# Kernel tuning notes

Hardware: AMD Instinct MI355X
Metric: run time of the kernel (lower is better)

## Reference

```python
import jax, jax.numpy as jnp
import numpy as np

# Qwen3-Next GatedDeltaNet dims (tp_size = 1)
H = 2048          # hidden_size
HK, HV = 16, 32   # num_k_heads, num_v_heads
G = HV // HK      # v-heads per k-head
DK, DV = 128, 128 # head_k_dim, head_v_dim
KEY_DIM = HK * DK        # 2048
VAL_DIM = HV * DV        # 4096
CONV_DIM = 2 * KEY_DIM + VAL_DIM   # 8192
QKVZ = 2 * KEY_DIM + 2 * VAL_DIM   # 12288
BA = 2 * HV
K = 4             # conv kernel size
L = 4096          # tokens (one prefill sequence)
EPS = 1e-6


def setup_inputs() -> dict:
    key = jax.random.key(0)
    ks = jax.random.split(key, 5)
    s = lambda k, shape, sc: jax.random.normal(k, shape, jnp.float32) * sc
    return {
        'hidden_states': s(ks[0], (L, H), 1.0),
        'in_proj_w': s(ks[1], (H, QKVZ + BA), H ** -0.5),
        'conv_w': s(ks[2], (CONV_DIM, K), 0.25),
        'A_log': jnp.zeros((HV,), jnp.float32),
        'dt_bias': jnp.ones((HV,), jnp.float32),
        'norm_w': jnp.ones((DV,), jnp.float32),
        'out_proj_w': s(ks[3], (VAL_DIM, H), VAL_DIM ** -0.5),
    }


def _l2norm(x):
    return x * jax.lax.rsqrt(jnp.sum(x * x, axis=-1, keepdims=True) + EPS)


def _gdn_forward(hidden_states, in_proj_w, conv_w, A_log, dt_bias, norm_w, out_proj_w):
    # in_proj -> split qkvz / ba, fix_query_key_value_ordering
    proj = hidden_states @ in_proj_w                       # [L, QKVZ+BA]
    qkvz, ba = proj[:, :QKVZ], proj[:, QKVZ:]
    qkvz = qkvz.reshape(L, HK, 2 * DK + 2 * G * DV)        # per-k-head layout
    q = qkvz[:, :, :DK]                                    # [L,HK,DK]
    k = qkvz[:, :, DK:2 * DK]                              # [L,HK,DK]
    v = qkvz[:, :, 2 * DK:2 * DK + G * DV].reshape(L, HV, DV)
    z = qkvz[:, :, 2 * DK + G * DV:].reshape(L, HV, DV)
    ba = ba.reshape(L, HK, 2 * G)
    b = ba[:, :, :G].reshape(L, HV)
    a = ba[:, :, G:].reshape(L, HV)

    # depthwise causal conv1d over time (kernel K, left pad K-1) + silu
    mixed_qkv = jnp.concatenate(
        [q.reshape(L, KEY_DIM), k.reshape(L, KEY_DIM), v.reshape(L, VAL_DIM)], axis=-1)
    xp = jnp.pad(mixed_qkv, ((K - 1, 0), (0, 0)))
    conv_out = sum(conv_w[:, j] * xp[j:j + L] for j in range(K))
    mixed_qkv = jax.nn.silu(conv_out)

    q = mixed_qkv[:, :KEY_DIM].reshape(L, HK, DK)
    k = mixed_qkv[:, KEY_DIM:2 * KEY_DIM].reshape(L, HK, DK)
    v = mixed_qkv[:, 2 * KEY_DIM:].reshape(L, HV, DV)

    # gating: beta = sigmoid(b); g = -exp(A_log) * softplus(a + dt_bias)
    beta = jax.nn.sigmoid(b)                               # [L,HV]
    g = -jnp.exp(A_log) * jax.nn.softplus(a + dt_bias)     # [L,HV] (log decay)

    # expand k-heads to v-heads, qk l2-norm, scale q
    q = jnp.repeat(q, G, axis=1)                           # [L,HV,DK]
    k = jnp.repeat(k, G, axis=1)
    q = _l2norm(q) * (DK ** -0.5)
    k = _l2norm(k)

    # gated delta rule recurrence over time (state S: [HV, DK, DV])
    def step(S, inp):
        q_t, k_t, v_t, g_t, b_t = inp
        S = S * jnp.exp(g_t)[:, None, None]
        delta = (v_t - jnp.einsum('hk,hkv->hv', k_t, S)) * b_t[:, None]
        S = S + jnp.einsum('hk,hv->hkv', k_t, delta)
        o = jnp.einsum('hk,hkv->hv', q_t, S)
        return S, o

    S0 = jnp.zeros((HV, DK, DV), jnp.float32)
    _, core = jax.lax.scan(step, S0, (q, k, v, g, beta))   # core: [L,HV,DV]

    # gated RMSNorm (norm before gate): RMSNorm(x)*w*silu(z)
    var = jnp.mean(core * core, axis=-1, keepdims=True)
    core = core * jax.lax.rsqrt(var + EPS) * norm_w
    core = core * jax.nn.silu(z)

    return core.reshape(L, VAL_DIM) @ out_proj_w           # [L, H]


def reference(hidden_states, in_proj_w, conv_w, A_log, dt_bias, norm_w, out_proj_w):
    return _gdn_forward(hidden_states, in_proj_w, conv_w, A_log, dt_bias, norm_w, out_proj_w)
```

## Files before the change

### kernel.cpp

```cpp
#include <hip/hip_runtime.h>
#include <hip/hip_bf16.h>

#define L_SEQ 4096
#define HDIM 2048
#define NPROJA 8256
#define NPACK 12352
#define WLD 12352
#define EPS_ 1e-6f

using bf16 = __hip_bfloat16;
typedef __attribute__((ext_vector_type(8))) short short8;
typedef __attribute__((ext_vector_type(4))) float f32x4;

__device__ __forceinline__ float b2f(bf16 x) { return __bfloat162float(x); }
__device__ __forceinline__ bf16 f2b(float x) { return __float2bfloat16(x); }
__device__ __forceinline__ unsigned short b2u(bf16 x) {
  union { bf16 b; unsigned short u; } c; c.b = x; return c.u;
}
__device__ __forceinline__ void* swz(void* base, int row, int rowbytes, int colbyte) {
  return (void*)((char*)base + row * rowbytes + (colbyte ^ ((row & 7) << 4)));
}
__device__ __forceinline__ const void* swzc(const void* base, int row, int rowbytes, int colbyte) {
  return (const void*)((const char*)base + row * rowbytes + (colbyte ^ ((row & 7) << 4)));
}
__device__ __forceinline__ void* swzk(void* base, int row, int colbyte) {
  return (void*)((char*)base + row * 128 + (colbyte ^ (((row >> 3) & 7) << 4)));
}
__device__ __forceinline__ const void* swzkc(const void* base, int row, int colbyte) {
  return (const void*)((const char*)base + row * 128 + (colbyte ^ (((row >> 3) & 7) << 4)));
}

__device__ __forceinline__ void async_copy16(const void* g, void* l) {
  __builtin_amdgcn_global_load_lds(
      (const __attribute__((address_space(1))) void*)g,
      (__attribute__((address_space(3))) void*)l, 16, 0, 0);
}

__global__ __launch_bounds__(256) void cvt_bf16(const float* __restrict__ in,
                                                bf16* __restrict__ outp) {
  int i = (blockIdx.x * 256 + threadIdx.x) * 4;
  float4 v = *(const float4*)&in[i];
  bf16 o4[4] = {f2b(v.x), f2b(v.y), f2b(v.z), f2b(v.w)};
  *(ushort4*)&outp[i] = *(ushort4*)o4;
}

template <int MODE>
__device__ __forceinline__ int pmap(int n) {
  if constexpr (MODE == 3) {
    if (n < 2048) return (n >> 7) * 768 + (n & 127);
    else if (n < 4096) { int m = n - 2048; return (m >> 7) * 768 + 128 + (m & 127); }
    else if (n < 8192) { int m = n - 4096; return (m >> 8) * 768 + 256 + (m & 255); }
    else if (n < 8256) return 12288 + (n - 8192);
    else { int m = n - 8256; return (m >> 8) * 768 + 512 + (m & 255); }
  } else {
    return n;
  }
}

template <int MODE>
__global__ __launch_bounds__(256) void transpose_w(
    const float* __restrict__ W, bf16* __restrict__ Bt, int ldw, int Kd) {
  __shared__ float T[64][65];
  const int nb = blockIdx.x * 64, kb = blockIdx.y * 64;
  const int tid = threadIdx.x;
  const int c = tid & 63, gq = tid >> 6;
  const int sbase = pmap<MODE>(nb);
#pragma unroll
  for (int i = 0; i < 16; ++i) {
    int r = gq * 16 + i;
    T[c][r] = W[(size_t)(kb + r) * ldw + sbase + c];
  }
  __syncthreads();
#pragma unroll
  for (int i = 0; i < 16; ++i) {
    int n = gq * 16 + i;
    Bt[(size_t)(nb + n) * Kd + kb + c] = f2b(T[n][c]);
  }
}

template <int ROUTE>
__global__ __launch_bounds__(256) void gemm_bt(
    const bf16* __restrict__ A, const bf16* __restrict__ Bt,
    void* __restrict__ Cp, bf16* __restrict__ Cz, int N, int Kd,
    int MBnum, int NBnum) {
  __shared__ bf16 As[2][128 * 32];
  __shared__ bf16 Bs[2][128 * 32];
  const int tid = threadIdx.x;
  const int wave = tid >> 6, lane = tid & 63;
  const int l15 = lane & 15, quad = lane >> 4;

  int m_blk, n_blk;
  {
    const int CW = 32;
    int fullc = NBnum / CW;
    int rem = NBnum - fullc * CW;
    int thr = fullc * CW * MBnum;
    int wg = blockIdx.x;
    if (wg < thr) {
      int cw = CW * MBnum;
      int chunk = wg / cw, w = wg - chunk * cw;
      n_blk = chunk * CW + (w & (CW - 1));
      m_blk = w / CW;
    } else {
      int w2 = wg - thr;
      int r = rem ? rem : 1;
      n_blk = fullc * CW + w2 % r;
      m_blk = w2 / r;
    }
  }
  const int m0 = m_blk * 128, n0 = n_blk * 128;
  const int mw = (wave >> 1) * 64, nw = (wave & 1) * 64;

  f32x4 acc[4][4];
#pragma unroll
  for (int i = 0; i < 4; i++)
#pragma unroll
    for (int j = 0; j < 4; j++) acc[i][j] = {0.f, 0.f, 0.f, 0.f};

  const bf16* a_src0 = A + (size_t)(m0 + (tid >> 2)) * Kd + (tid & 3) * 8;
  const bf16* a_src1 = a_src0 + (size_t)64 * Kd;
  const bf16* b_src0 = Bt + (size_t)(n0 + (tid >> 2)) * Kd + (tid & 3) * 8;
  const bf16* b_src1 = b_src0 + (size_t)64 * Kd;
  const int d0 = tid * 8, d1 = (tid + 256) * 8;

  async_copy16(a_src0, &As[0][d0]);
  async_copy16(a_src1, &As[0][d1]);
  async_copy16(b_src0, &Bs[0][d0]);
  async_copy16(b_src1, &Bs[0][d1]);

  int cur = 0;
  for (int k0 = 0; k0 < Kd; k0 += 32, cur ^= 1) {
    __syncthreads();
    if (k0 + 32 < Kd) {
      const int nk = k0 + 32, nb = cur ^ 1;
      async_copy16(a_src0 + nk, &As[nb][d0]);
      async_copy16(a_src1 + nk, &As[nb][d1]);
      async_copy16(b_src0 + nk, &Bs[nb][d0]);
      async_copy16(b_src1 + nk, &Bs[nb][d1]);
    }
    short8 af[4], bfr[4];
#pragma unroll
    for (int i = 0; i < 4; i++)
      af[i] = *(const short8*)&As[cur][(mw + i * 16 + l15) * 32 + quad * 8];
#pragma unroll
    for (int j = 0; j < 4; j++)
      bfr[j] = *(const short8*)&Bs[cur][(nw + j * 16 + l15) * 32 + quad * 8];
#pragma unroll
    for (int i = 0; i < 4; i++)
#pragma unroll
      for (int j = 0; j < 4; j++)
        acc[i][j] = __builtin_amdgcn_mfma_f32_16x16x32_bf16(af[i], bfr[j],
                                                            acc[i][j], 0, 0, 0);
  }

#pragma unroll
  for (int i = 0; i < 4; i++) {
#pragma unroll
    for (int j = 0; j < 4; j++) {
      int col = n0 + nw + j * 16 + l15;
      if (col < N) {
#pragma unroll
        for (int r = 0; r < 4; r++) {
          int row = m0 + mw + i * 16 + quad * 4 + r;
          if (ROUTE == 0) {
            ((float*)Cp)[(size_t)row * N + col] = acc[i][j][r];
          } else {
            if (col < NPROJA)
              ((bf16*)Cp)[(size_t)row * NPROJA + col] = f2b(acc[i][j][r]);
            else
              Cz[(size_t)row * 4096 + (col - NPROJA)] = f2b(acc[i][j][r]);
          }
        }
      }
    }
  }
}

__global__ __launch_bounds__(128) void conv_norm_qk(
    const bf16* __restrict__ proj, const float* __restrict__ conv_w,
    bf16* __restrict__ qn, bf16* __restrict__ kn) {
  const int t = blockIdx.x >> 4, hk = blockIdx.x & 15;
  const int d = threadIdx.x;
  const int cq = hk * 128 + d;
  const int ck = 2048 + hk * 128 + d;
  float sq = 0.f, sk = 0.f;
#pragma unroll
  for (int j = 0; j < 4; j++) {
    int ts = t + j - 3;
    if (ts >= 0) {
      sq += conv_w[cq * 4 + j] * b2f(proj[(size_t)ts * NPROJA + cq]);
      sk += conv_w[ck * 4 + j] * b2f(proj[(size_t)ts * NPROJA + ck]);
    }
  }
  float qv = sq / (1.f + expf(-sq));
  float kv = sk / (1.f + expf(-sk));
  float ssq = qv * qv, ssk = kv * kv;
#pragma unroll
  for (int off = 32; off > 0; off >>= 1) {
    ssq += __shfl_down(ssq, off, 64);
    ssk += __shfl_down(ssk, off, 64);
  }
  __shared__ float red[4];
  if ((d & 63) == 0) {
    red[(d >> 6) * 2] = ssq;
    red[(d >> 6) * 2 + 1] = ssk;
  }
  __syncthreads();
  float sumq = red[0] + red[2];
  float sumk = red[1] + red[3];
  size_t o = (size_t)(t * 16 + hk) * 128 + d;
  qn[o] = f2b(qv * rsqrtf(sumq + EPS_) * 0.08838834764831845f);
  kn[o] = f2b(kv * rsqrtf(sumk + EPS_));
}

__global__ __launch_bounds__(256) void conv_silu_v(
    const bf16* __restrict__ proj, const float* __restrict__ conv_w,
    bf16* __restrict__ vbuf) {
  int idx = blockIdx.x * 256 + threadIdx.x;
  int t = idx >> 12, c = idx & 4095;
  int chan = 4096 + c;
  float s = 0.f;
#pragma unroll
  for (int j = 0; j < 4; j++) {
    int ts = t + j - 3;
    if (ts >= 0) s += conv_w[chan * 4 + j] * b2f(proj[(size_t)ts * NPROJA + chan]);
  }
  vbuf[idx] = f2b(s / (1.f + expf(-s)));
}

__global__ __launch_bounds__(256) void compute_bg(
    const bf16* __restrict__ proj, const float* __restrict__ A_log,
    const float* __restrict__ dt_bias, float* __restrict__ beta_arr,
    float* __restrict__ g_arr) {
  int idx = blockIdx.x * 256 + threadIdx.x;
  int t = idx >> 5, hv = idx & 31;
  size_t base = (size_t)t * NPROJA + 8192 + (hv >> 1) * 4 + (hv & 1);
  float b = b2f(proj[base]);
  float a = b2f(proj[base + 2]);
  beta_arr[idx] = 1.f / (1.f + expf(-b));
  float x = a + dt_bias[hv];
  float sp = (x > 20.f) ? x : log1pf(expf(x));
  g_arr[idx] = -expf(A_log[hv]) * sp;
}

__global__ __launch_bounds__(512) void precompute_chunk(
    const bf16* __restrict__ kn, const bf16* __restrict__ vbuf,
    const float* __restrict__ g_arr, const float* __restrict__ beta_arr,
    bf16* __restrict__ TV, bf16* __restrict__ TK) {
  const int c = blockIdx.x >> 5, h = blockIdx.x & 31, hk = h >> 1;
  const int t0 = c * 64, tid = threadIdx.x;
  __shared__ float Kf[64][129];
  __shared__ float X[64][256];
  __shared__ float BA[64][64];
  __shared__ float cgs[64], bet[64], eKs[64];

  for (int e = tid; e < 1024; e += 512) {
    int row = e >> 4, s = e & 15;
    short8 v = *(const short8*)(kn + ((size_t)(t0 + row) * 16 + hk) * 128 + s * 8);
    bf16 tmp[8];
    *(short8*)tmp = v;
#pragma unroll
    for (int k = 0; k < 8; ++k) Kf[row][s * 8 + k] = b2f(tmp[k]);
  }
  if (tid < 64) {
    float bb = beta_arr[(size_t)(t0 + tid) * 32 + h];
    bet[tid] = bb;
    float x = g_arr[(size_t)(t0 + tid) * 32 + h];
#pragma unroll
    for (int off = 1; off < 64; off <<= 1) {
      float o = __shfl_up(x, off, 64);
      if (tid >= off) x += o;
    }
    cgs[tid] = x;
    eKs[tid] = bb * expf(x);
  }
  __syncthreads();
  for (int e = tid; e < 8192; e += 512) {
    int i = e >> 7, d = e & 127;
    X[i][d] = bet[i] * b2f(vbuf[(size_t)(t0 + i) * 4096 + h * 128 + d]);
    X[i][128 + d] = eKs[i] * Kf[i][d];
  }
  {
    const int ti = tid >> 4, tj = tid & 15;
    float acc[2][4];
#pragma unroll
    for (int r = 0; r < 2; ++r)
#pragma unroll
      for (int s = 0; s < 4; ++s) acc[r][s] = 0.f;
    for (int dk = 0; dk < 128; ++dk) {
      float a0 = Kf[ti * 2 + 0][dk], a1 = Kf[ti * 2 + 1][dk];
      float c0 = Kf[tj * 4 + 0][dk], c1 = Kf[tj * 4 + 1][dk];
      float c2 = Kf[tj * 4 + 2][dk], c3 = Kf[tj * 4 + 3][dk];
      acc[0][0] += a0 * c0; acc[0][1] += a0 * c1; acc[0][2] += a0 * c2; acc[0][3] += a0 * c3;
      acc[1][0] += a1 * c0; acc[1][1] += a1 * c1; acc[1][2] += a1 * c2; acc[1][3] += a1 * c3;
    }
#pragma unroll
    for (int r = 0; r < 2; ++r)
#pragma unroll
      for (int s = 0; s < 4; ++s) {
        int i = ti * 2 + r, j = tj * 4 + s;
        BA[i][j] = (j < i) ? bet[i] * expf(cgs[i] - cgs[j]) * acc[r][s] : 0.f;
      }
  }
  __syncthreads();
  if (tid < 256) {
    const int d = tid;
    for (int i = 1; i < 64; ++i) {
      const float* bar = BA[i];
      float s0 = 0.f, s1 = 0.f;
      int j = 0;
      for (; j + 1 < i; j += 2) {
        s0 += bar[j] * X[j][d];
        s1 += bar[j + 1] * X[j + 1][d];
      }
      if (j < i) s0 += bar[j] * X[j][d];
      X[i][d] -= s0 + s1;
    }
  }
  __syncthreads();
  for (int e = tid; e < 8192; e += 512) {
    int i = e >> 7, d = e & 127;
    size_t o = ((size_t)(t0 + i) * 32 + h) * 128 + d;
    TV[o] = f2b(X[i][d]);
    TK[o] = f2b(X[i][128 + d]);
  }
}

__global__ __launch_bounds__(512) void seq_kernel(
    bf16* TVU,
    const bf16* __restrict__ TKg, const bf16* __restrict__ qn,
    const bf16* __restrict__ kn, const float* __restrict__ g_arr,
    bf16* __restrict__ Oin) {
  const int h = blockIdx.x >> 1, dvh = blockIdx.x & 1, hk = h >> 1;
  const int dv0 = dvh * 64;
  const int tid = threadIdx.x;
  const int wave = tid >> 6, lane = tid & 63, l15 = lane & 15, quad = lane >> 4;
  const int mi = wave >> 1, half = wave & 1;
  const int srow = tid >> 4, scol = tid & 15;

  __shared__ bf16 STh[64 * 128], STl[64 * 128];
  __shared__ bf16 UTh[64 * 64], UTl[64 * 64];
  __shared__ bf16 TKs[64 * 128];
  __shared__ bf16 Qts[64 * 128];
  __shared__ bf16 KhT[128 * 64];

  for (int e = tid; e < 4096; e += 512) {
    ((unsigned int*)STh)[e] = 0u;
    ((unsigned int*)STl)[e] = 0u;
  }
  f32x4 Sf[4];
#pragma unroll
  for (int i = 0; i < 4; i++) Sf[i] = {0.f, 0.f, 0.f, 0.f};

  short8 tkr0, tkr1, qr0, qr1, kr0, kr1;
  float gv;
  auto issue_loads = [&](int c) {
    const size_t t0 = (size_t)c << 6;
    tkr0 = *(const short8*)(TKg + ((t0 + srow) * 32 + h) * 128 + scol * 8);
    tkr1 = *(const short8*)(TKg + ((t0 + 32 + srow) * 32 + h) * 128 + scol * 8);
    qr0 = *(const short8*)(qn + ((t0 + srow) * 16 + hk) * 128 + scol * 8);
    qr1 = *(const short8*)(qn + ((t0 + 32 + srow) * 16 + hk) * 128 + scol * 8);
    kr0 = *(const short8*)(kn + ((t0 + srow) * 16 + hk) * 128 + scol * 8);
    kr1 = *(const short8*)(kn + ((t0 + 32 + srow) * 16 + hk) * 128 + scol * 8);
    gv = g_arr[(t0 + lane) * 32 + h];
  };
  issue_loads(0);

  for (int c = 0; c < 64; ++c) {
    const int t0 = c << 6;
    __syncthreads();

    bf16 tvp[2][4];
#pragma unroll
    for (int nj = 0; nj < 2; nj++) {
      const int nrow = half * 32 + nj * 16 + l15;
#pragma unroll
      for (int r = 0; r < 4; r++) {
        const int i = mi * 16 + quad * 4 + r;
        tvp[nj][r] = TVU[((size_t)(t0 + i) * 32 + h) * 128 + dv0 + nrow];
      }
    }
    float cg = gv;
#pragma unroll
    for (int off = 1; off < 64; off <<= 1) {
      float o = __shfl_up(cg, off, 64);
      if (lane >= off) cg += o;
    }
    const float cg63 = __shfl(cg, 63, 64);
    const float lam = expf(cg63);
    const float fq = expf(cg);
    const float fk = expf(cg63 - cg);
    *(short8*)swz(TKs, srow, 256, scol * 16) = tkr0;
    *(short8*)swz(TKs, srow + 32, 256, scol * 16) = tkr1;
    {
      const float f0 = __shfl(fq, srow, 64);
      const float f1 = __shfl(fq, srow + 32, 64);
      bf16 ta[8], tb[8];
      *(short8*)ta = qr0;
      *(short8*)tb = qr1;
#pragma unroll
      for (int k = 0; k < 8; k++) {
        ta[k] = f2b(b2f(ta[k]) * f0);
        tb[k] = f2b(b2f(tb[k]) * f1);
      }
      *(short8*)swz(Qts, srow, 256, scol * 16) = *(short8*)ta;
      *(short8*)swz(Qts, srow + 32, 256, scol * 16) = *(short8*)tb;
    }
    {
      const float f0 = __shfl(fk, srow, 64);
      const float f1 = __shfl(fk, srow + 32, 64);
      bf16 ka[8], kb[8];
      *(short8*)ka = kr0;
      *(short8*)kb = kr1;
#pragma unroll
      for (int k = 0; k < 8; k++) {
        const int dk = scol * 8 + k;
        *(bf16*)swzk(KhT, dk, srow * 2) = f2b(b2f(ka[k]) * f0);
        *(bf16*)swzk(KhT, dk, (srow + 32) * 2) = f2b(b2f(kb[k]) * f1);
      }
    }
    issue_loads(c + 1 < 64 ? c + 1 : 63);
    __syncthreads();

    f32x4 oacc[2], xacc[2];
#pragma unroll
    for (int nj = 0; nj < 2; nj++) { oacc[nj] = {0.f,0.f,0.f,0.f}; xacc[nj] = {0.f,0.f,0.f,0.f}; }
    const int arow = mi * 16 + l15;
#pragma unroll
    for (int ks = 0; ks < 4; ++ks) {
      const int cb = ks * 64 + quad * 16;
      short8 aq = *(const short8*)swzc(Qts, arow, 256, cb);
      short8 at = *(const short8*)swzc(TKs, arow, 256, cb);
#pragma unroll
      for (int nj = 0; nj < 2; nj++) {
        const int nrow = half * 32 + nj * 16 + l15;
        short8 bh = *(const short8*)swzc(STh, nrow, 256, cb);
        short8 bl = *(const short8*)swzc(STl, nrow, 256, cb);
        oacc[nj] = __builtin_amdgcn_mfma_f32_16x16x32_bf16(aq, bh, oacc[nj], 0, 0, 0);
        xacc[nj] = __builtin_amdgcn_mfma_f32_16x16x32_bf16(at, bh, xacc[nj], 0, 0, 0);
        xacc[nj] = __builtin_amdgcn_mfma_f32_16x16x32_bf16(at, bl, xacc[nj], 0, 0, 0);
      }
    }
    const int krow = wave * 16 + l15;
    short8 ak0 = *(const short8*)swzkc(KhT, krow, 0 * 64 + quad * 16);
    short8 ak1 = *(const short8*)swzkc(KhT, krow, 1 * 64 + quad * 16);

#pragma unroll
    for (int nj = 0; nj < 2; nj++) {
      const int nrow = half * 32 + nj * 16 + l15;
      unsigned short ph[4], pl[4];
#pragma unroll
      for (int r = 0; r < 4; ++r) {
        const int i = mi * 16 + quad * 4 + r;
        const size_t go = ((size_t)(t0 + i) * 32 + h) * 128 + dv0 + nrow;
        Oin[go] = f2b(oacc[nj][r]);
        float uv = b2f(tvp[nj][r]) - xacc[nj][r];
        bf16 hb = f2b(uv);
        TVU[go] = hb;
        ph[r] = b2u(hb);
        pl[r] = b2u(f2b(uv - b2f(hb)));
      }
      const int cb = (mi * 16 + quad * 4) * 2;
      ushort4 vh; vh.x = ph[0]; vh.y = ph[1]; vh.z = ph[2]; vh.w = ph[3];
      ushort4 vl; vl.x = pl[0]; vl.y = pl[1]; vl.z = pl[2]; vl.w = pl[3];
      *(ushort4*)swz(UTh, nrow, 128, cb) = vh;
      *(ushort4*)swz(UTl, nrow, 128, cb) = vl;
    }
    __syncthreads();

#pragma unroll
    for (int nj = 0; nj < 4; nj++) {
      Sf[nj][0] *= lam; Sf[nj][1] *= lam; Sf[nj][2] *= lam; Sf[nj][3] *= lam;
    }
#pragma unroll
    for (int ks = 0; ks < 2; ++ks) {
      const short8 ak = ks ? ak1 : ak0;
      const int cb = ks * 64 + quad * 16;
#pragma unroll
      for (int nj = 0; nj < 4; nj++) {
        const int nrow = nj * 16 + l15;
        short8 bh = *(const short8*)swzc(UTh, nrow, 128, cb);
        short8 bl = *(const short8*)swzc(UTl, nrow, 128, cb);
        Sf[nj] = __builtin_amdgcn_mfma_f32_16x16x32_bf16(ak, bh, Sf[nj], 0, 0, 0);
        Sf[nj] = __builtin_amdgcn_mfma_f32_16x16x32_bf16(ak, bl, Sf[nj], 0, 0, 0);
      }
    }
#pragma unroll
    for (int nj = 0; nj < 4; nj++) {
      const int nrow = nj * 16 + l15;
      unsigned short ph[4], pl[4];
#pragma unroll
      for (int r = 0; r < 4; ++r) {
        float s = Sf[nj][r];
        bf16 hb = f2b(s);
        ph[r] = b2u(hb);
        pl[r] = b2u(f2b(s - b2f(hb)));
      }
      const int cb = (wave * 16 + quad * 4) * 2;
      ushort4 vh; vh.x = ph[0]; vh.y = ph[1]; vh.z = ph[2]; vh.w = ph[3];
      ushort4 vl; vl.x = pl[0]; vl.y = pl[1]; vl.z = pl[2]; vl.w = pl[3];
      *(ushort4*)swz(STh, nrow, 256, cb) = vh;
      *(ushort4*)swz(STl, nrow, 256, cb) = vl;
    }
  }
}

__global__ __launch_bounds__(512) void pass2_kernel(
    bf16* UC,
    const bf16* __restrict__ Oin, const bf16* __restrict__ qn,
    const bf16* __restrict__ kn, const float* __restrict__ g_arr,
    const bf16* __restrict__ zbuf, const float* __restrict__ norm_w) {
  const int c = blockIdx.x >> 5, h = blockIdx.x & 31, hk = h >> 1;
  const int t0 = c * 64, tid = threadIdx.x;
  __shared__ float Qf[64][129], Kf[64][129];
  __shared__ float Uf[64][128];
  __shared__ float Of[64][129];
  __shared__ float At[64][65];
  __shared__ float cgs[64], nw[128];

  for (int e = tid; e < 1024; e += 512) {
    int row = e >> 4, s = e & 15;
    size_t qko = ((size_t)(t0 + row) * 16 + hk) * 128 + s * 8;
    size_t uo = ((size_t)(t0 + row) * 32 + h) * 128 + s * 8;
    short8 vq = *(const short8*)(qn + qko);
    short8 vk = *(const short8*)(kn + qko);
    short8 vu = *(const short8*)(UC + uo);
    short8 vo = *(const short8*)(Oin + uo);
    bf16 tq[8], tk[8], tu[8], to[8];
    *(short8*)tq = vq; *(short8*)tk = vk; *(short8*)tu = vu; *(short8*)to = vo;
#pragma unroll
    for (int k = 0; k < 8; ++k) {
      Qf[row][s * 8 + k] = b2f(tq[k]);
      Kf[row][s * 8 + k] = b2f(tk[k]);
      Uf[row][s * 8 + k] = b2f(tu[k]);
      Of[row][s * 8 + k] = b2f(to[k]);
    }
  }
  if (tid < 64) {
    float x = g_arr[(size_t)(t0 + tid) * 32 + h];
#pragma unroll
    for (int off = 1; off < 64; off <<= 1) {
      float o = __shfl_up(x, off, 64);
      if (tid >= off) x += o;
    }
    cgs[tid] = x;
  }
  if (tid < 128) nw[tid] = norm_w[tid];
  __syncthreads();
  {
    const int ti = tid >> 4, tj = tid & 15;
    float acc[2][4];
#pragma unroll
    for (int r = 0; r < 2; ++r)
#pragma unroll
      for (int s = 0; s < 4; ++s) acc[r][s] = 0.f;
    for (int dk = 0; dk < 128; ++dk) {
      float a0 = Qf[ti * 2 + 0][dk], a1 = Qf[ti * 2 + 1][dk];
      float c0 = Kf[tj * 4 + 0][dk], c1 = Kf[tj * 4 + 1][dk];
      float c2 = Kf[tj * 4 + 2][dk], c3 = Kf[tj * 4 + 3][dk];
      acc[0][0] += a0 * c0; acc[0][1] += a0 * c1; acc[0][2] += a0 * c2; acc[0][3] += a0 * c3;
      acc[1][0] += a1 * c0; acc[1][1] += a1 * c1; acc[1][2] += a1 * c2; acc[1][3] += a1 * c3;
    }
#pragma unroll
    for (int r = 0; r < 2; ++r)
#pragma unroll
      for (int s = 0; s < 4; ++s) {
        int i = ti * 2 + r, j = tj * 4 + s;
        At[i][j] = (j <= i) ? expf(cgs[i] - cgs[j]) * acc[r][s] : 0.f;
      }
  }
  __syncthreads();
  {
    const int ri = tid >> 4, tn = tid & 15;
    float acc[2][8];
#pragma unroll
    for (int r = 0; r < 2; ++r)
#pragma unroll
      for (int k = 0; k < 8; ++k) acc[r][k] = 0.f;
    for (int j = 0; j < 64; ++j) {
      float a0 = At[ri * 2 + 0][j], a1 = At[ri * 2 + 1][j];
#pragma unroll
      for (int k = 0; k < 8; ++k) {
        float u = Uf[j][tn + 16 * k];
        acc[0][k] += a0 * u;
        acc[1][k] += a1 * u;
      }
    }
#pragma unroll
    for (int r = 0; r < 2; ++r)
#pragma unroll
      for (int k = 0; k < 8; ++k)
        Of[ri * 2 + r][tn + 16 * k] += acc[r][k];
  }
  __syncthreads();
  {
    const int r = tid >> 3, q8 = tid & 7;
    float ss = 0.f;
#pragma unroll
    for (int k = 0; k < 16; ++k) {
      float v = Of[r][q8 + 8 * k];
      ss += v * v;
    }
    ss += __shfl_xor(ss, 1, 64);
    ss += __shfl_xor(ss, 2, 64);
    ss += __shfl_xor(ss, 4, 64);
    float scale = rsqrtf(ss * (1.f / 128.f) + EPS_);
#pragma unroll
    for (int k = 0; k < 16; ++k) {
      int n = q8 + 8 * k;
      float val = Of[r][n] * scale * nw[n];
      float zz = b2f(zbuf[(size_t)(t0 + r) * 4096 + h * 128 + n]);
      val *= zz / (1.f + expf(-zz));
      UC[((size_t)(t0 + r) * 32 + h) * 128 + n] = f2b(val);
    }
  }
}

extern "C" void kernel_launch(void* const* d_in, const int* in_sizes, int n_in,
                              void* d_out, int out_size, void* d_ws,
                              size_t ws_size, hipStream_t stream) {
  const float* hidden = (const float*)d_in[0];
  const float* in_w = (const float*)d_in[1];
  const float* conv_w = (const float*)d_in[2];
  const float* A_log = (const float*)d_in[3];
  const float* dt_bias = (const float*)d_in[4];
  const float* norm_w = (const float*)d_in[5];
  const float* out_w = (const float*)d_in[6];
  float* out = (float*)d_out;

  char* p = (char*)d_ws;
  bf16* projA = (bf16*)p;
  bf16* TV = (bf16*)p;
  bf16* TK = (bf16*)(p + 33554432ULL);
  bf16* zbuf = (bf16*)(p + 67633152ULL);
  char* pR = p + 101187584ULL;
  bf16* vbuf = (bf16*)pR;
  float* beta = (float*)(pR + 33554432ULL);
  float* g = (float*)(pR + 34078720ULL);
  bf16* qn = (bf16*)(pR + 34603008ULL);
  bf16* kn = (bf16*)(pR + 51380224ULL);
  bf16* Bt_in = (bf16*)pR;
  bf16* hb16 = (bf16*)(pR + 50659328ULL);
  bf16* Bt_out = (bf16*)zbuf;

  cvt_bf16<<<(L_SEQ * HDIM) / 1024, 256, 0, stream>>>(hidden, hb16);
  transpose_w<3><<<dim3(193, 32), 256, 0, stream>>>(in_w, Bt_in, WLD, HDIM);
  gemm_bt<1><<<97 * 32, 256, 0, stream>>>(hb16, Bt_in, projA, zbuf,
                                          NPACK, HDIM, 32, 97);
  conv_norm_qk<<<L_SEQ * 16, 128, 0, stream>>>(projA, conv_w, qn, kn);
  conv_silu_v<<<(L_SEQ * 4096) / 256, 256, 0, stream>>>(projA, conv_w, vbuf);
  compute_bg<<<(L_SEQ * 32) / 256, 256, 0, stream>>>(projA, A_log, dt_bias,
                                                     beta, g);
  precompute_chunk<<<2048, 512, 0, stream>>>(kn, vbuf, g, beta, TV, TK);
  seq_kernel<<<64, 512, 0, stream>>>(TV, TK, qn, kn, g, vbuf);
  pass2_kernel<<<2048, 512, 0, stream>>>(TV, vbuf, qn, kn, g, zbuf, norm_w);
  transpose_w<0><<<dim3(32, 64), 256, 0, stream>>>(out_w, Bt_out, 2048, 4096);
  gemm_bt<0><<<16 * 32, 256, 0, stream>>>(TV, Bt_out, out, nullptr,
                                          2048, 4096, 32, 16);
}
```

Baseline: 1.393 ms.

## Use MFMA for chunk K·Kᵀ and blocked triangular solve in precompute_chunk

Keys are kept in swizzled bf16 shared memory, and the strictly-lower 64x64 K·Kᵀ block is computed with 16x16x32 bf16 MFMA instructions instead of scalar fp32 FMAs. The forward-substitution solve is split into 16-row blocks: a parallel block update across all 512 threads, then a short serial in-block solve. Loads of V and K into X are vectorized. The aim is to cut scalar work and the long serial dependency chain in the per-chunk WY precompute. In exchange it adds more barriers, and the K·Kᵀ products now rely on bf16 inputs with fp32 accumulation.

```diff
diff --git a/kernel.cpp b/kernel.cpp
--- a/kernel.cpp
+++ b/kernel.cpp
@@ -249,18 +249,18 @@
     bf16* __restrict__ TV, bf16* __restrict__ TK) {
   const int c = blockIdx.x >> 5, h = blockIdx.x & 31, hk = h >> 1;
   const int t0 = c * 64, tid = threadIdx.x;
-  __shared__ float Kf[64][129];
+  const int wave = tid >> 6, lane = tid & 63, l15 = lane & 15, quad = lane >> 4;
+  __shared__ bf16 Ks[64 * 128];
   __shared__ float X[64][256];
-  __shared__ float BA[64][64];
+  __shared__ float BA[64][65];
   __shared__ float cgs[64], bet[64], eKs[64];
 
-  for (int e = tid; e < 1024; e += 512) {
-    int row = e >> 4, s = e & 15;
-    short8 v = *(const short8*)(kn + ((size_t)(t0 + row) * 16 + hk) * 128 + s * 8);
-    bf16 tmp[8];
-    *(short8*)tmp = v;
-#pragma unroll
-    for (int k = 0; k < 8; ++k) Kf[row][s * 8 + k] = b2f(tmp[k]);
+  {
+    const int row = tid >> 4, s = tid & 15;
+    short8 v0 = *(const short8*)(kn + ((size_t)(t0 + row) * 16 + hk) * 128 + s * 8);
+    short8 v1 = *(const short8*)(kn + ((size_t)(t0 + 32 + row) * 16 + hk) * 128 + s * 8);
+    *(short8*)swz(Ks, row, 256, s * 16) = v0;
+    *(short8*)swz(Ks, row + 32, 256, s * 16) = v1;
   }
   if (tid < 64) {
     float bb = beta_arr[(size_t)(t0 + tid) * 32 + h];
@@ -275,46 +275,82 @@
     eKs[tid] = bb * expf(x);
   }
   __syncthreads();
-  for (int e = tid; e < 8192; e += 512) {
-    int i = e >> 7, d = e & 127;
-    X[i][d] = bet[i] * b2f(vbuf[(size_t)(t0 + i) * 4096 + h * 128 + d]);
-    X[i][128 + d] = eKs[i] * Kf[i][d];
+
+#pragma unroll
+  for (int s = 0; s < 2; ++s) {
+    const int b = wave * 2 + s, bi = b >> 2, bj = b & 3;
+    if (bi >= bj) {
+      f32x4 acc = {0.f, 0.f, 0.f, 0.f};
+      const int ar = bi * 16 + l15, br = bj * 16 + l15;
+#pragma unroll
+      for (int ks = 0; ks < 4; ++ks) {
+        const int cb = ks * 64 + quad * 16;
+        short8 af = *(const short8*)swzc(Ks, ar, 256, cb);
+        short8 bf = *(const short8*)swzc(Ks, br, 256, cb);
+        acc = __builtin_amdgcn_mfma_f32_16x16x32_bf16(af, bf, acc, 0, 0, 0);
+      }
+#pragma unroll
+      for (int r = 0; r < 4; ++r) {
+        const int i = bi * 16 + quad * 4 + r, j = bj * 16 + l15;
+        if (j < i) BA[i][j] = bet[i] * expf(cgs[i] - cgs[j]) * acc[r];
+      }
+    }
   }
   {
-    const int ti = tid >> 4, tj = tid & 15;
-    float acc[2][4];
-#pragma unroll
-    for (int r = 0; r < 2; ++r)
-#pragma unroll
-      for (int s = 0; s < 4; ++s) acc[r][s] = 0.f;
-    for (int dk = 0; dk < 128; ++dk) {
-      float a0 = Kf[ti * 2 + 0][dk], a1 = Kf[ti * 2 + 1][dk];
-      float c0 = Kf[tj * 4 + 0][dk], c1 = Kf[tj * 4 + 1][dk];
-      float c2 = Kf[tj * 4 + 2][dk], c3 = Kf[tj * 4 + 3][dk];
-      acc[0][0] += a0 * c0; acc[0][1] += a0 * c1; acc[0][2] += a0 * c2; acc[0][3] += a0 * c3;
-      acc[1][0] += a1 * c0; acc[1][1] += a1 * c1; acc[1][2] += a1 * c2; acc[1][3] += a1 * c3;
-    }
-#pragma unroll
-    for (int r = 0; r < 2; ++r)
-#pragma unroll
-      for (int s = 0; s < 4; ++s) {
-        int i = ti * 2 + r, j = tj * 4 + s;
-        BA[i][j] = (j < i) ? bet[i] * expf(cgs[i] - cgs[j]) * acc[r][s] : 0.f;
-      }
-  }
-  __syncthreads();
-  if (tid < 256) {
-    const int d = tid;
-    for (int i = 1; i < 64; ++i) {
-      const float* bar = BA[i];
-      float s0 = 0.f, s1 = 0.f;
-      int j = 0;
-      for (; j + 1 < i; j += 2) {
-        s0 += bar[j] * X[j][d];
-        s1 += bar[j + 1] * X[j + 1][d];
-      }
-      if (j < i) s0 += bar[j] * X[j][d];
-      X[i][d] -= s0 + s1;
+    const int i = tid >> 4, s = tid & 15;
+#pragma unroll
+    for (int half = 0; half < 2; ++half) {
+      const int row = i + half * 32;
+      short8 vv = *(const short8*)(vbuf + (size_t)(t0 + row) * 4096 + h * 128 + s * 8);
+      short8 kv = *(const short8*)swzc(Ks, row, 256, s * 16);
+      bf16 tv_[8], tk_[8];
+      *(short8*)tv_ = vv;
+      *(short8*)tk_ = kv;
+      const float bb = bet[row], ee = eKs[row];
+      float o0[8], o1[8];
+#pragma unroll
+      for (int k = 0; k < 8; ++k) {
+        o0[k] = bb * b2f(tv_[k]);
+        o1[k] = ee * b2f(tk_[k]);
+      }
+      *(float4*)&X[row][s * 8] = *(float4*)&o0[0];
+      *(float4*)&X[row][s * 8 + 4] = *(float4*)&o0[4];
+      *(float4*)&X[row][128 + s * 8] = *(float4*)&o1[0];
+      *(float4*)&X[row][128 + s * 8 + 4] = *(float4*)&o1[4];
+    }
+  }
+
+  const int li = tid >> 5, g4 = (tid & 31) * 4;
+#pragma unroll
+  for (int t = 0; t < 4; ++t) {
+    const int i0 = t * 16;
+    __syncthreads();
+    if (t > 0) {
+      const int gi = i0 + li;
+      float4 a0 = *(float4*)&X[gi][g4];
+      float4 a1 = *(float4*)&X[gi][128 + g4];
+      for (int j = 0; j < i0; ++j) {
+        const float bij = BA[gi][j];
+        float4 x0 = *(float4*)&X[j][g4];
+        float4 x1 = *(float4*)&X[j][128 + g4];
+        a0.x -= bij * x0.x; a0.y -= bij * x0.y;
+        a0.z -= bij * x0.z; a0.w -= bij * x0.w;
+        a1.x -= bij * x1.x; a1.y -= bij * x1.y;
+        a1.z -= bij * x1.z; a1.w -= bij * x1.w;
+      }
+      *(float4*)&X[gi][g4] = a0;
+      *(float4*)&X[gi][128 + g4] = a1;
+      __syncthreads();
+    }
+    if (tid < 256) {
+      const int d = tid;
+#pragma unroll
+      for (int i2 = 1; i2 < 16; ++i2) {
+        const int i = i0 + i2;
+        float s = 0.f;
+        for (int j = i0; j < i; ++j) s += BA[i][j] * X[j][d];
+        X[i][d] -= s;
+      }
     }
   }
   __syncthreads();
```

New measurement: 1.170 ms. 16.0% less time.
